# Optimization experiments

Measured on AMD Instinct MI355X. Metric: run time of the kernel, lower is better.

Reference implementation:

```python
import jax, jax.numpy as jnp
import numpy as np

N_HEAD = 8
HID = 256
V_DIM = HID // N_HEAD
IN_CH = 3
OUT_CH = 1
N_BLOCKS = 4
BATCH = 4
N_FULL = 4096
N_LAT = 1024
LOCALITIES = (3.0, 5.0, 5.0, 5.0, 5.0, 3.0)


def _linear(x, w, b):
    # eqx.nn.Linear convention: w is [out, in]
    return x @ w.T + b


def _pos_att(m_dist, x, r, weight, locality):
    # m_dist: [h, Nq, Nk]; x: [b, Nk, HID]; r: [h,1,1]; weight: [h, HID, V_DIM]
    scale = jnp.tan(0.25 * jnp.pi * (1 - 1e-07) * (1 + jnp.sin(r)))  # [h,1,1]
    sd = m_dist * scale  # [h, Nq, Nk]
    if locality <= 100:
        thr = jnp.percentile(sd, locality, axis=-1, keepdims=True)
        sd = jnp.where(sd <= thr, sd, jnp.inf)
    att = jax.nn.softmax(-sd, axis=-1)  # [h, Nq, Nk]
    value = jnp.einsum('bnj,hjk->bhnk', x, weight)  # [b, h, Nk, V_DIM]
    out = jnp.einsum('hjn,bhnk->bhjk', att, value)  # [b, h, Nq, V_DIM]
    out = out.transpose(0, 2, 1, 3).reshape(out.shape[0], out.shape[2], -1)  # [b, Nq, HID]
    return jax.nn.gelu(out)


def setup_inputs():
    key = jax.random.key(0)
    ks = jax.random.split(key, 16)
    def nrm(k, shape, scale=1.0):
        return jax.random.normal(k, shape, dtype=jnp.float32) * scale
    inv = float(1.0 / np.sqrt(HID))
    return {
        'x': nrm(ks[0], (BATCH, N_FULL, IN_CH)),
        'm_dist_down': jax.random.uniform(ks[1], (N_HEAD, N_LAT, N_FULL), dtype=jnp.float32),
        'm_dist_blocks': jax.random.uniform(ks[2], (N_BLOCKS, N_HEAD, N_LAT, N_LAT), dtype=jnp.float32),
        'm_dist_up': jax.random.uniform(ks[3], (N_HEAD, N_FULL, N_LAT), dtype=jnp.float32),
        'en_w': nrm(ks[4], (HID, IN_CH), float(1.0 / np.sqrt(IN_CH))),
        'en_b': jnp.zeros((HID,), jnp.float32),
        'down_r': nrm(ks[5], (N_HEAD, 1, 1)),
        'down_w': nrm(ks[6], (N_HEAD, HID, V_DIM), inv),
        'pa_r': nrm(ks[7], (N_BLOCKS, N_HEAD, 1, 1)),
        'pa_w': nrm(ks[8], (N_BLOCKS, N_HEAD, HID, V_DIM), inv),
        'mlp1_w': nrm(ks[9], (N_BLOCKS, HID, HID), inv),
        'mlp1_b': jnp.zeros((N_BLOCKS, HID), jnp.float32),
        'mlp2_w': nrm(ks[10], (N_BLOCKS, HID, HID), inv),
        'mlp2_b': jnp.zeros((N_BLOCKS, HID), jnp.float32),
        'res_w': nrm(ks[11], (N_BLOCKS, HID, HID), inv),
        'res_b': jnp.zeros((N_BLOCKS, HID), jnp.float32),
        'up_r': nrm(ks[12], (N_HEAD, 1, 1)),
        'up_w': nrm(ks[13], (N_HEAD, HID, V_DIM), inv),
        'de1_w': nrm(ks[14], (HID, HID), inv),
        'de1_b': jnp.zeros((HID,), jnp.float32),
        'de2_w': nrm(ks[15], (OUT_CH, HID), inv),
        'de2_b': jnp.zeros((OUT_CH,), jnp.float32),
    }


def reference(x, m_dist_down, m_dist_blocks, m_dist_up, en_w, en_b, down_r, down_w,
              pa_r, pa_w, mlp1_w, mlp1_b, mlp2_w, mlp2_b, res_w, res_b,
              up_r, up_w, de1_w, de1_b, de2_w, de2_b):
    # Encoder: lift + downsampling position-attention
    h = jax.nn.gelu(_linear(x, en_w, en_b))  # [b, N_FULL, HID]
    h = _pos_att(m_dist_down, h, down_r, down_w, LOCALITIES[0])  # [b, N_LAT, HID]
    # Processor blocks: PA -> MLP, plus linear residual, gelu
    for i in range(N_BLOCKS):
        pa = _pos_att(m_dist_blocks[i], h, pa_r[i], pa_w[i], LOCALITIES[1 + i])
        mlp = _linear(jax.nn.gelu(_linear(pa, mlp1_w[i], mlp1_b[i])), mlp2_w[i], mlp2_b[i])
        h = jax.nn.gelu(mlp + _linear(h, res_w[i], res_b[i]))
    # Decoder: upsampling position-attention + projection
    h = _pos_att(m_dist_up, h, up_r, up_w, LOCALITIES[-1])  # [b, N_FULL, HID]
    h = jax.nn.gelu(_linear(h, de1_w, de1_b))
    return _linear(h, de2_w, de2_b)  # [b, N_FULL, OUT_CH]
```

## Files before the change

### kernel.cpp

```cpp
#include <hip/hip_runtime.h>
#include <math.h>


typedef short bf16x8 __attribute__((ext_vector_type(8)));
typedef float f32x4 __attribute__((ext_vector_type(4)));

__device__ __forceinline__ float gelu_f(float x) {
  float x3 = x * x * x;
  float inner = x + 0.044715f * x3;
  float t = tanhf(0.7978845608028654f * inner);
  return x * (0.5f * (1.0f + t));
}

__device__ __forceinline__ unsigned short f2bf(float x) {
  union { float f; unsigned u; } v; v.f = x;
  return (unsigned short)((v.u + 0x7fffu + ((v.u >> 16) & 1u)) >> 16);
}
__device__ __forceinline__ float bf2f(unsigned short b) {
  union { unsigned u; float f; } v; v.u = ((unsigned)b) << 16; return v.f;
}
__device__ __forceinline__ void store_bf(unsigned short* hi, unsigned short* lo,
                                         size_t i, float v) {
  unsigned short h = f2bf(v);
  hi[i] = h;
  lo[i] = f2bf(v - bf2f(h));
}

struct PrepArgs {
  const float *mlp1, *mlp2, *res, *de1, *down, *pa, *up;
  const float *down_r, *pa_r, *up_r;
  unsigned short *rm_hi, *rm_lo, *val_hi, *val_lo;
  float* scales;
};
__global__ __launch_bounds__(256) void k_prep(PrepArgs p) {
  if (blockIdx.x == 4864) {
    int t = threadIdx.x;
    if (t >= 48) return;
    float rv;
    if (t < 8) rv = p.down_r[t];
    else if (t < 40) rv = p.pa_r[t - 8];
    else rv = p.up_r[t - 40];
    double rd = (double)rv;
    float s1 = (float)sin(rd);
    float u = 1.0f + s1;
    float vc = (float)(0.7853981633974483 * (1.0 - 1e-7));
    float wf = vc * u;
    p.scales[t] = (float)tan((double)wf);
    return;
  }
  int i = blockIdx.x * 256 + threadIdx.x;
  if (i < 851968) {
    const float* src; int off;
    if (i < 262144)      { src = p.mlp1; off = i; }
    else if (i < 524288) { src = p.mlp2; off = i - 262144; }
    else if (i < 786432) { src = p.res;  off = i - 524288; }
    else                 { src = p.de1;  off = i - 786432; }
    float x = src[off];
    store_bf(p.rm_hi, p.rm_lo, i, x);
  } else if (i < 1245184) {
    int ii = i - 851968;
    const float* src; int off;
    if (ii < 65536)       { src = p.down; off = ii; }
    else if (ii < 327680) { src = p.pa;   off = ii - 65536; }
    else                  { src = p.up;   off = ii - 327680; }
    int m = off >> 16, rem = off & 65535;
    int o = rem >> 8, j = rem & 255;
    float x = src[(size_t)m * 65536 + (o >> 5) * 8192 + j * 32 + (o & 31)];
    store_bf(p.val_hi, p.val_lo, ii, x);
  }
}

__global__ __launch_bounds__(256) void k_lift(const float* __restrict__ x,
                                              const float* __restrict__ w,
                                              const float* __restrict__ b,
                                              unsigned short* __restrict__ ohi,
                                              unsigned short* __restrict__ olo) {
  int gid = blockIdx.x * 256 + threadIdx.x;
  int m = gid >> 8, o = gid & 255;
  float a0 = x[m * 3 + 0], a1 = x[m * 3 + 1], a2 = x[m * 3 + 2];
  float acc = a0 * w[o * 3 + 0] + a1 * w[o * 3 + 1] + a2 * w[o * 3 + 2] + b[o];
  store_bf(ohi, olo, gid, gelu_f(acc));
}

template <int ACT, int ADDRES, int OBF16>
__global__ __launch_bounds__(256) void k_gemm(
    const unsigned short* __restrict__ Ahi, const unsigned short* __restrict__ Alo,
    const unsigned short* __restrict__ Whi, const unsigned short* __restrict__ Wlo,
    const float* __restrict__ bias, const float* __restrict__ D,
    float* __restrict__ C, unsigned short* __restrict__ Chi,
    unsigned short* __restrict__ Clo) {
  int t = threadIdx.x;
  int w = t >> 6, l = t & 63;
  int m0 = blockIdx.x * 64 + (w >> 1) * 32;
  int o0 = blockIdx.y * 64 + (w & 1) * 32;
  int fr = l & 15, fq = l >> 4;
  f32x4 acc[2][2] = {};
  size_t a0 = (size_t)(m0 + fr) * 256 + fq * 8;
  size_t a1 = a0 + 16 * 256;
  size_t b0 = (size_t)(o0 + fr) * 256 + fq * 8;
  size_t b1 = b0 + 16 * 256;
#define MFMA4(ACC, AH, AL, BH, BL)                                            \
  ACC = __builtin_amdgcn_mfma_f32_16x16x32_bf16(AH, BH, ACC, 0, 0, 0);        \
  ACC = __builtin_amdgcn_mfma_f32_16x16x32_bf16(AH, BL, ACC, 0, 0, 0);        \
  ACC = __builtin_amdgcn_mfma_f32_16x16x32_bf16(AL, BH, ACC, 0, 0, 0);        \
  ACC = __builtin_amdgcn_mfma_f32_16x16x32_bf16(AL, BL, ACC, 0, 0, 0);
  for (int ks = 0; ks < 8; ++ks) {
    int k0 = ks * 32;
    bf16x8 A0h = *(const bf16x8*)(Ahi + a0 + k0);
    bf16x8 A0l = *(const bf16x8*)(Alo + a0 + k0);
    bf16x8 A1h = *(const bf16x8*)(Ahi + a1 + k0);
    bf16x8 A1l = *(const bf16x8*)(Alo + a1 + k0);
    bf16x8 B0h = *(const bf16x8*)(Whi + b0 + k0);
    bf16x8 B0l = *(const bf16x8*)(Wlo + b0 + k0);
    bf16x8 B1h = *(const bf16x8*)(Whi + b1 + k0);
    bf16x8 B1l = *(const bf16x8*)(Wlo + b1 + k0);
    MFMA4(acc[0][0], A0h, A0l, B0h, B0l)
    MFMA4(acc[0][1], A0h, A0l, B1h, B1l)
    MFMA4(acc[1][0], A1h, A1l, B0h, B0l)
    MFMA4(acc[1][1], A1h, A1l, B1h, B1l)
  }
  float bb[2];
  bb[0] = bias ? bias[o0 + fr] : 0.0f;
  bb[1] = bias ? bias[o0 + 16 + fr] : 0.0f;
#pragma unroll
  for (int i = 0; i < 2; ++i) {
#pragma unroll
    for (int jx = 0; jx < 2; ++jx) {
      int col = o0 + jx * 16 + fr;
#pragma unroll
      for (int r = 0; r < 4; ++r) {
        int rowi = m0 + i * 16 + fq * 4 + r;
        size_t oidx = (size_t)rowi * 256 + col;
        float v = acc[i][jx][r] + bb[jx];
        if (ADDRES) v += D[oidx];
        if (ACT) v = gelu_f(v);
        if (OBF16) store_bf(Chi, Clo, oidx, v);
        else C[oidx] = v;
      }
    }
  }
}

__global__ __launch_bounds__(256) void k_gemm2(
    const unsigned short* __restrict__ A1hi, const unsigned short* __restrict__ A1lo,
    const unsigned short* __restrict__ W1hi, const unsigned short* __restrict__ W1lo,
    const unsigned short* __restrict__ A2hi, const unsigned short* __restrict__ A2lo,
    const unsigned short* __restrict__ W2hi, const unsigned short* __restrict__ W2lo,
    const float* __restrict__ b1, const float* __restrict__ b2,
    unsigned short* __restrict__ Chi, unsigned short* __restrict__ Clo) {
  int t = threadIdx.x;
  int w = t >> 6, l = t & 63;
  int m0 = blockIdx.x * 64 + (w >> 1) * 32;
  int o0 = blockIdx.y * 64 + (w & 1) * 32;
  int fr = l & 15, fq = l >> 4;
  f32x4 acc[2][2] = {};
  size_t a0 = (size_t)(m0 + fr) * 256 + fq * 8;
  size_t a1 = a0 + 16 * 256;
  size_t b0 = (size_t)(o0 + fr) * 256 + fq * 8;
  size_t b1o = b0 + 16 * 256;
  for (int ks = 0; ks < 8; ++ks) {
    int k0 = ks * 32;
    {
      bf16x8 A0h = *(const bf16x8*)(A1hi + a0 + k0);
      bf16x8 A0l = *(const bf16x8*)(A1lo + a0 + k0);
      bf16x8 A1h_ = *(const bf16x8*)(A1hi + a1 + k0);
      bf16x8 A1l_ = *(const bf16x8*)(A1lo + a1 + k0);
      bf16x8 B0h = *(const bf16x8*)(W1hi + b0 + k0);
      bf16x8 B0l = *(const bf16x8*)(W1lo + b0 + k0);
      bf16x8 B1h = *(const bf16x8*)(W1hi + b1o + k0);
      bf16x8 B1l = *(const bf16x8*)(W1lo + b1o + k0);
      MFMA4(acc[0][0], A0h, A0l, B0h, B0l)
      MFMA4(acc[0][1], A0h, A0l, B1h, B1l)
      MFMA4(acc[1][0], A1h_, A1l_, B0h, B0l)
      MFMA4(acc[1][1], A1h_, A1l_, B1h, B1l)
    }
    {
      bf16x8 A0h = *(const bf16x8*)(A2hi + a0 + k0);
      bf16x8 A0l = *(const bf16x8*)(A2lo + a0 + k0);
      bf16x8 A1h_ = *(const bf16x8*)(A2hi + a1 + k0);
      bf16x8 A1l_ = *(const bf16x8*)(A2lo + a1 + k0);
      bf16x8 B0h = *(const bf16x8*)(W2hi + b0 + k0);
      bf16x8 B0l = *(const bf16x8*)(W2lo + b0 + k0);
      bf16x8 B1h = *(const bf16x8*)(W2hi + b1o + k0);
      bf16x8 B1l = *(const bf16x8*)(W2lo + b1o + k0);
      MFMA4(acc[0][0], A0h, A0l, B0h, B0l)
      MFMA4(acc[0][1], A0h, A0l, B1h, B1l)
      MFMA4(acc[1][0], A1h_, A1l_, B0h, B0l)
      MFMA4(acc[1][1], A1h_, A1l_, B1h, B1l)
    }
  }
#undef MFMA4
  float bb[2];
  bb[0] = b1[o0 + fr] + b2[o0 + fr];
  bb[1] = b1[o0 + 16 + fr] + b2[o0 + 16 + fr];
#pragma unroll
  for (int i = 0; i < 2; ++i) {
#pragma unroll
    for (int jx = 0; jx < 2; ++jx) {
      int col = o0 + jx * 16 + fr;
#pragma unroll
      for (int r = 0; r < 4; ++r) {
        int rowi = m0 + i * 16 + fq * 4 + r;
        size_t oidx = (size_t)rowi * 256 + col;
        store_bf(Chi, Clo, oidx, gelu_f(acc[i][jx][r] + bb[jx]));
      }
    }
  }
}

template <int N, int CAP, int MW>
__global__ __launch_bounds__(256, MW) void k_wselpv(
    const float* __restrict__ mdist, const float* __restrict__ scales,
    int sc_off, int Nq, int k_lo, float hw, float lw, float frac,
    const float* __restrict__ V, int Nk,
    unsigned short* __restrict__ out_hi, unsigned short* __restrict__ out_lo) {
  constexpr int CH = N / 256;
  constexpr int SMAX = (CAP + 63) / 64;
  __shared__ float cv[4][CAP];
  __shared__ int ci[4][CAP];
  __shared__ int ccnt[4];
  __shared__ float svsel[4][2];
  __shared__ float swin[4][32];

  int tid = threadIdx.x;
  int w = tid >> 6, l = tid & 63;
  int row = blockIdx.x * 4 + w;
  int h = row / Nq, j = row - h * Nq;
  float scale = scales[sc_off + h];
  const float4* mrow4 = (const float4*)(mdist + (size_t)row * N);

  float4 s0 = mrow4[l];
  float smin = fminf(fminf(s0.x, s0.y), fminf(s0.z, s0.w));
  float smax = fmaxf(fmaxf(s0.x, s0.y), fmaxf(s0.z, s0.w));
#pragma unroll
  for (int off = 32; off > 0; off >>= 1) {
    smin = fminf(smin, __shfl_xor(smin, off));
    smax = fmaxf(smax, __shfl_xor(smax, off));
  }
  float est = smin + (smax - smin) * frac;

  if (l == 0) ccnt[w] = 0;
  float lmin = INFINITY, lmax = -INFINITY;
#pragma unroll 4
  for (int e = 0; e < CH; ++e) {
    float4 v = mrow4[l + 64 * e];
    lmin = fminf(lmin, fminf(fminf(v.x, v.y), fminf(v.z, v.w)));
    lmax = fmaxf(lmax, fmaxf(fmaxf(v.x, v.y), fmaxf(v.z, v.w)));
    int i0 = 4 * (l + 64 * e);
    if (v.x < est) { int p = atomicAdd(&ccnt[w], 1); if (p < CAP) { cv[w][p] = v.x; ci[w][p] = i0; } }
    if (v.y < est) { int p = atomicAdd(&ccnt[w], 1); if (p < CAP) { cv[w][p] = v.y; ci[w][p] = i0 + 1; } }
    if (v.z < est) { int p = atomicAdd(&ccnt[w], 1); if (p < CAP) { cv[w][p] = v.z; ci[w][p] = i0 + 2; } }
    if (v.w < est) { int p = atomicAdd(&ccnt[w], 1); if (p < CAP) { cv[w][p] = v.w; ci[w][p] = i0 + 3; } }
  }
#pragma unroll
  for (int off = 32; off > 0; off >>= 1) {
    lmin = fminf(lmin, __shfl_xor(lmin, off));
    lmax = fmaxf(lmax, __shfl_xor(lmax, off));
  }
  float rmin = lmin, rmax = lmax;

  int K = 0;
  float inv_total = 1.0f;
  if (rmax > rmin) {
    float range = rmax - rmin;
    float margin = fmaxf(fabsf(rmax) * 1e-6f, 1e-30f);
    float rtop = rmax + margin;
    float wtop = est;
    bool have = true;
    if (!(wtop > rmin)) {
      wtop = rmin + range * frac;
      if (!(wtop > rmin)) wtop = rtop;
      have = false;
    }
    int attempt = 0;
    float v_lo = rmin, v_hi = rmin;
    int count = 0;
    float xv[SMAX];
    for (int it = 0; it < 20; ++it) {
      if (!have) {
        if (l == 0) ccnt[w] = 0;
#pragma unroll 4
        for (int e = 0; e < CH; ++e) {
          float4 v = mrow4[l + 64 * e];
          int i0 = 4 * (l + 64 * e);
          if (v.x < wtop) { int p = atomicAdd(&ccnt[w], 1); if (p < CAP) { cv[w][p] = v.x; ci[w][p] = i0; } }
          if (v.y < wtop) { int p = atomicAdd(&ccnt[w], 1); if (p < CAP) { cv[w][p] = v.y; ci[w][p] = i0 + 1; } }
          if (v.z < wtop) { int p = atomicAdd(&ccnt[w], 1); if (p < CAP) { cv[w][p] = v.z; ci[w][p] = i0 + 2; } }
          if (v.w < wtop) { int p = atomicAdd(&ccnt[w], 1); if (p < CAP) { cv[w][p] = v.w; ci[w][p] = i0 + 3; } }
        }
        have = true;
      }
      count = ccnt[w];
      if (count < k_lo + 2) {
        wtop = (attempt == 0) ? (rmin + range * frac)
                              : fminf(rmin + (wtop - rmin) * 3.0f, rtop);
        if (!(wtop > rmin)) wtop = rtop;
        attempt++; have = false; continue;
      }
      if (count > CAP) {
        float fw = rmin + range * frac;
        float sw = rmin + (wtop - rmin) * 0.6f;
        wtop = (attempt == 0) ? fminf(fw, sw) : sw;
        attempt++; have = false; continue;
      }

#pragma unroll
      for (int s = 0; s < SMAX; ++s) {
        int slot = l + 64 * s;
        xv[s] = (slot < count) ? cv[w][slot] : INFINITY;
      }
      float wlo = rmin, whi = wtop;
      int rbase = 0, cntw = count;
      int found = 0, degen = 0;
      for (int bs = 0; bs < 32; ++bs) {
        if (cntw <= 24) break;
        float mid = 0.5f * (wlo + whi);
        if (!(mid > wlo && mid < whi)) { degen = 1; break; }
        int c4 = 0;
#pragma unroll
        for (int s = 0; s < SMAX; ++s) c4 += (xv[s] >= wlo && xv[s] < mid) ? 1 : 0;
#pragma unroll
        for (int off = 32; off > 0; off >>= 1) c4 += __shfl_xor(c4, off);
        int rrel = k_lo - rbase;
        if (rrel + 1 < c4) { whi = mid; cntw = c4; }
        else if (rrel >= c4) { wlo = mid; rbase += c4; cntw -= c4; }
        else {
          float mx = -INFINITY, mn = INFINITY;
#pragma unroll
          for (int s = 0; s < SMAX; ++s) {
            float v = xv[s];
            if (v >= wlo && v < mid) mx = fmaxf(mx, v);
            if (v >= mid && v < whi) mn = fminf(mn, v);
          }
#pragma unroll
          for (int off = 32; off > 0; off >>= 1) {
            mx = fmaxf(mx, __shfl_xor(mx, off));
            mn = fminf(mn, __shfl_xor(mn, off));
          }
          v_lo = mx; v_hi = mn; found = 1;
          break;
        }
      }
      if (!found) {
        if (!degen && cntw <= 32) {
          if (l == 0) ccnt[w] = 0;
#pragma unroll
          for (int s = 0; s < SMAX; ++s) {
            float v = xv[s];
            if (v >= wlo && v < whi) {
              int p = atomicAdd(&ccnt[w], 1);
              if (p < 32) swin[w][p] = v;
            }
          }
          int m = ccnt[w];
          if (m > 32) m = 32;
          float myv = (l < m) ? swin[w][l] : INFINITY;
          int clt = 0, ceq = 0;
          for (int jj = 0; jj < m; ++jj) {
            float y = swin[w][jj];
            clt += (y < myv) ? 1 : 0;
            ceq += (y == myv) ? 1 : 0;
          }
          int rr = k_lo - rbase;
          if (l < m) {
            if (clt <= rr && rr < clt + ceq) svsel[w][0] = myv;
            if (clt <= rr + 1 && rr + 1 < clt + ceq) svsel[w][1] = myv;
          }
          v_lo = svsel[w][0];
          v_hi = svsel[w][1];
          if (l == 0) ccnt[w] = count;
        } else {
          int clt[SMAX], ceq[SMAX];
#pragma unroll
          for (int s = 0; s < SMAX; ++s) { clt[s] = 0; ceq[s] = 0; }
          for (int jj = 0; jj < count; ++jj) {
            float y = cv[w][jj];
#pragma unroll
            for (int s = 0; s < SMAX; ++s) {
              clt[s] += (y < xv[s]) ? 1 : 0;
              ceq[s] += (y == xv[s]) ? 1 : 0;
            }
          }
#pragma unroll
          for (int s = 0; s < SMAX; ++s) {
            int slot = l + 64 * s;
            if (slot < count) {
              if (clt[s] <= k_lo && k_lo < clt[s] + ceq[s]) svsel[w][0] = xv[s];
              if (clt[s] <= k_lo + 1 && k_lo + 1 < clt[s] + ceq[s]) svsel[w][1] = xv[s];
            }
          }
          v_lo = svsel[w][0];
          v_hi = svsel[w][1];
        }
      }
      float vlos0 = __fmul_rn(v_lo, scale);
      float vhis0 = __fmul_rn(v_hi, scale);
      float thr0 = __fadd_rn(__fmul_rn(vlos0, lw), __fmul_rn(vhis0, hw));
      if (__fmul_rn(wtop, scale) <= thr0) {
        wtop = fminf(rmin + (wtop - rmin) * 3.0f, rtop);
        attempt++; have = false; continue;
      }
      break;
    }

    float vlos = __fmul_rn(v_lo, scale);
    float vhis = __fmul_rn(v_hi, scale);
    float thr = __fadd_rn(__fmul_rn(vlos, lw), __fmul_rn(vhis, hw));
    float rmins = __fmul_rn(rmin, scale);

    int oi[SMAX]; int kp[SMAX];
#pragma unroll
    for (int s = 0; s < SMAX; ++s) {
      int slot = l + 64 * s;
      oi[s] = 0; kp[s] = 0;
      if (slot < count) {
        oi[s] = ci[w][slot];
        kp[s] = (__fmul_rn(xv[s], scale) <= thr) ? 1 : 0;
      }
    }
    int base = 0;
    float lsum = 0.0f;
    unsigned long long mlt = (l == 0) ? 0ull : (~0ull >> (64 - l));
#pragma unroll
    for (int s = 0; s < SMAX; ++s) {
      unsigned long long bal = __ballot(kp[s] != 0);
      int pos = base + (int)__popcll(bal & mlt);
      if (kp[s]) {
        float e0 = expf(__fsub_rn(rmins, __fmul_rn(xv[s], scale)));
        cv[w][pos] = e0;
        ci[w][pos] = oi[s];
        lsum += e0;
      }
      base += (int)__popcll(bal);
    }
    K = base;
#pragma unroll
    for (int off = 32; off > 0; off >>= 1) lsum += __shfl_xor(lsum, off);
    inv_total = 1.0f / lsum;
  } else {
    K = 0;
    inv_total = 1.0f / (float)Nk;
  }

  int b = l >> 4, c4 = (l & 15) * 2;
  int hcol = h * 32 + c4;
  const float* Vb = V + (size_t)b * Nk * 256;
  float acc0 = 0.0f, acc1 = 0.0f;
  if (K > 0) {
    for (int e = 0; e < K; ++e) {
      float we = cv[w][e];
      int n = ci[w][e];
      const float2 vv = *(const float2*)(Vb + (size_t)n * 256 + hcol);
      acc0 = fmaf(we, vv.x, acc0);
      acc1 = fmaf(we, vv.y, acc1);
    }
  } else {
    for (int n = 0; n < Nk; ++n) {
      const float2 vv = *(const float2*)(Vb + (size_t)n * 256 + hcol);
      acc0 += vv.x;
      acc1 += vv.y;
    }
  }
  size_t oidx = ((size_t)b * Nq + j) * 256 + hcol;
  store_bf(out_hi, out_lo, oidx, gelu_f(acc0 * inv_total));
  store_bf(out_hi, out_lo, oidx + 1, gelu_f(acc1 * inv_total));
}

__global__ __launch_bounds__(256) void k_de2(const float* __restrict__ A,
                                             const float* __restrict__ w,
                                             const float* __restrict__ b,
                                             float* __restrict__ out) {
  int t = threadIdx.x;
  int row = blockIdx.x * 4 + (t >> 6);
  int lane = t & 63;
  const float* ar = A + (size_t)row * 256;
  float s = 0.0f;
  for (int i = lane; i < 256; i += 64) s = fmaf(ar[i], w[i], s);
#pragma unroll
  for (int off = 32; off > 0; off >>= 1) s += __shfl_down(s, off);
  if (lane == 0) out[row] = s + b[0];
}

struct SelParams { int k_lo; float hw, lw, frac; };
static SelParams sel_params(double q, int N) {
  SelParams p;
  float idx_q = (float)(q / 100.0);
  float pos = idx_q * (float)(N - 1);
  float lo = floorf(pos);
  p.k_lo = (int)lo;
  p.hw = pos - lo;
  p.lw = 1.0f - p.hw;
  float need = (float)(p.k_lo + 2);
  p.frac = (need + 6.0f * sqrtf(need) + 8.0f) / (float)N;
  return p;
}

extern "C" void kernel_launch(void* const* d_in, const int* in_sizes, int n_in,
                              void* d_out, int out_size, void* d_ws, size_t ws_size,
                              hipStream_t stream) {
  const float* x      = (const float*)d_in[0];
  const float* mdd    = (const float*)d_in[1];
  const float* mdb    = (const float*)d_in[2];
  const float* mdu    = (const float*)d_in[3];
  const float* en_w   = (const float*)d_in[4];
  const float* en_b   = (const float*)d_in[5];
  const float* down_r = (const float*)d_in[6];
  const float* down_w = (const float*)d_in[7];
  const float* pa_r   = (const float*)d_in[8];
  const float* pa_w   = (const float*)d_in[9];
  const float* mlp1_w = (const float*)d_in[10];
  const float* mlp1_b = (const float*)d_in[11];
  const float* mlp2_w = (const float*)d_in[12];
  const float* mlp2_b = (const float*)d_in[13];
  const float* res_w  = (const float*)d_in[14];
  const float* res_b  = (const float*)d_in[15];
  const float* up_r   = (const float*)d_in[16];
  const float* up_w   = (const float*)d_in[17];
  const float* de1_w  = (const float*)d_in[18];
  const float* de1_b  = (const float*)d_in[19];
  const float* de2_w  = (const float*)d_in[20];
  const float* de2_b  = (const float*)d_in[21];
  float* out = (float*)d_out;
  char* base = (char*)d_ws;

  float* val               = (float*)base;
  unsigned short* hB_hi    = (unsigned short*)(base + 16777216);
  unsigned short* hB_lo    = (unsigned short*)(base + 18874368);
  unsigned short* hfull_hi = (unsigned short*)(base + 20971520);
  unsigned short* hfull_lo = (unsigned short*)(base + 29360128);
  unsigned short* paout_hi = (unsigned short*)(base + 37748736);
  unsigned short* paout_lo = (unsigned short*)(base + 46137344);
  unsigned short* hA_hi    = (unsigned short*)(base + 54525952);
  unsigned short* hA_lo    = (unsigned short*)(base + 56623104);
  unsigned short* t1_hi    = (unsigned short*)(base + 58720256);
  unsigned short* t1_lo    = (unsigned short*)(base + 60817408);
  unsigned short* wrm_hi   = (unsigned short*)(base + 62914560);
  unsigned short* wrm_lo   = (unsigned short*)(base + 64618496);
  unsigned short* wval_hi  = (unsigned short*)(base + 66322432);
  unsigned short* wval_lo  = (unsigned short*)(base + 67108864);
  float* scales            = (float*)(base + 67895296);

  PrepArgs pa;
  pa.mlp1 = mlp1_w; pa.mlp2 = mlp2_w; pa.res = res_w; pa.de1 = de1_w;
  pa.down = down_w; pa.pa = pa_w; pa.up = up_w;
  pa.down_r = down_r; pa.pa_r = pa_r; pa.up_r = up_r;
  pa.rm_hi = wrm_hi; pa.rm_lo = wrm_lo; pa.val_hi = wval_hi; pa.val_lo = wval_lo;
  pa.scales = scales;
  k_prep<<<4865, 256, 0, stream>>>(pa);

  k_lift<<<16384, 256, 0, stream>>>(x, en_w, en_b, hfull_hi, hfull_lo);

  SelParams pd = sel_params(3.0, 4096);
  k_gemm<0, 0, 0><<<dim3(256, 4), 256, 0, stream>>>(
      hfull_hi, hfull_lo, wval_hi, wval_lo, nullptr, nullptr, val, nullptr, nullptr);
  k_wselpv<4096, 256, 4><<<2048, 256, 0, stream>>>(
      mdd, scales, 0, 1024, pd.k_lo, pd.hw, pd.lw, pd.frac, val, 4096, hA_hi, hA_lo);

  SelParams pb = sel_params(5.0, 1024);
  for (int i = 0; i < 4; i++) {
    unsigned short* in_hi  = (i & 1) ? hB_hi : hA_hi;
    unsigned short* in_lo  = (i & 1) ? hB_lo : hA_lo;
    unsigned short* out_hi = (i & 1) ? hA_hi : hB_hi;
    unsigned short* out_lo = (i & 1) ? hA_lo : hB_lo;
    k_gemm<0, 0, 0><<<dim3(64, 4), 256, 0, stream>>>(
        in_hi, in_lo, wval_hi + 65536 + i * 65536, wval_lo + 65536 + i * 65536,
        nullptr, nullptr, val, nullptr, nullptr);
    k_wselpv<1024, 256, 8><<<2048, 256, 0, stream>>>(
        mdb + (size_t)i * 8388608, scales, 8 + i * 8, 1024, pb.k_lo, pb.hw, pb.lw,
        pb.frac, val, 1024, paout_hi, paout_lo);
    k_gemm<1, 0, 1><<<dim3(64, 4), 256, 0, stream>>>(
        paout_hi, paout_lo, wrm_hi + i * 65536, wrm_lo + i * 65536,
        mlp1_b + i * 256, nullptr, nullptr, t1_hi, t1_lo);
    k_gemm2<<<dim3(64, 4), 256, 0, stream>>>(
        t1_hi, t1_lo, wrm_hi + 262144 + i * 65536, wrm_lo + 262144 + i * 65536,
        in_hi, in_lo, wrm_hi + 524288 + i * 65536, wrm_lo + 524288 + i * 65536,
        mlp2_b + i * 256, res_b + i * 256, out_hi, out_lo);
  }

  SelParams pu = sel_params(3.0, 1024);
  k_gemm<0, 0, 0><<<dim3(64, 4), 256, 0, stream>>>(
      hA_hi, hA_lo, wval_hi + 327680, wval_lo + 327680, nullptr, nullptr,
      val, nullptr, nullptr);
  k_wselpv<1024, 192, 8><<<8192, 256, 0, stream>>>(
      mdu, scales, 40, 4096, pu.k_lo, pu.hw, pu.lw, pu.frac, val, 1024,
      paout_hi, paout_lo);

  k_gemm<1, 0, 0><<<dim3(256, 4), 256, 0, stream>>>(
      paout_hi, paout_lo, wrm_hi + 786432, wrm_lo + 786432, de1_b, nullptr,
      val, nullptr, nullptr);
  k_de2<<<4096, 256, 0, stream>>>(val, de2_w, de2_b, out);
}
```

Measured before the change: 521.7 us.

## Process each attention row with a whole block instead of one wavefront

Replaces the per-wavefront row selection kernel with a block-per-row version. All four wavefronts scan a quarter of the row, collect candidates into per-wave segments, wave 0 does the percentile search, and the weighted value gather is split across waves and reduced through shared memory. The initial candidate fraction margin is also tightened, which makes candidate sets smaller but may trigger more retry passes. The change adds block-wide barriers and runs 4x more blocks, and wave 0 becomes a serial bottleneck during selection.

```diff
diff --git a/kernel.cpp b/kernel.cpp
--- a/kernel.cpp
+++ b/kernel.cpp
@@ -208,262 +208,252 @@
   }
 }
 
-template <int N, int CAP, int MW>
-__global__ __launch_bounds__(256, MW) void k_wselpv(
+template <int N>
+__global__ __launch_bounds__(256, 8) void k_bselpv(
     const float* __restrict__ mdist, const float* __restrict__ scales,
     int sc_off, int Nq, int k_lo, float hw, float lw, float frac,
     const float* __restrict__ V, int Nk,
     unsigned short* __restrict__ out_hi, unsigned short* __restrict__ out_lo) {
-  constexpr int CH = N / 256;
-  constexpr int SMAX = (CAP + 63) / 64;
-  __shared__ float cv[4][CAP];
-  __shared__ int ci[4][CAP];
+  constexpr int CH = N / 1024;
+  constexpr int SEG = 64;
+  constexpr int CAP = 256;
+  __shared__ float cv[CAP];
+  __shared__ int ci[CAP];
   __shared__ int ccnt[4];
-  __shared__ float svsel[4][2];
-  __shared__ float swin[4][32];
-
-  int tid = threadIdx.x;
-  int w = tid >> 6, l = tid & 63;
-  int row = blockIdx.x * 4 + w;
+  __shared__ float sminmax[8];
+  __shared__ float svsel[2];
+  __shared__ float swin[32];
+  __shared__ int sgc;
+  __shared__ int sK;
+  __shared__ float sinv;
+  __shared__ int sflag;
+  __shared__ float2 pacc[256];
+
+  int t = threadIdx.x;
+  int w = t >> 6, l = t & 63;
+  int row = blockIdx.x;
   int h = row / Nq, j = row - h * Nq;
   float scale = scales[sc_off + h];
   const float4* mrow4 = (const float4*)(mdist + (size_t)row * N);
 
-  float4 s0 = mrow4[l];
-  float smin = fminf(fminf(s0.x, s0.y), fminf(s0.z, s0.w));
-  float smax = fmaxf(fmaxf(s0.x, s0.y), fmaxf(s0.z, s0.w));
-#pragma unroll
-  for (int off = 32; off > 0; off >>= 1) {
-    smin = fminf(smin, __shfl_xor(smin, off));
-    smax = fmaxf(smax, __shfl_xor(smax, off));
-  }
-  float est = smin + (smax - smin) * frac;
-
-  if (l == 0) ccnt[w] = 0;
   float lmin = INFINITY, lmax = -INFINITY;
-#pragma unroll 4
+#pragma unroll
   for (int e = 0; e < CH; ++e) {
-    float4 v = mrow4[l + 64 * e];
+    float4 v = mrow4[t + 256 * e];
     lmin = fminf(lmin, fminf(fminf(v.x, v.y), fminf(v.z, v.w)));
     lmax = fmaxf(lmax, fmaxf(fmaxf(v.x, v.y), fmaxf(v.z, v.w)));
-    int i0 = 4 * (l + 64 * e);
-    if (v.x < est) { int p = atomicAdd(&ccnt[w], 1); if (p < CAP) { cv[w][p] = v.x; ci[w][p] = i0; } }
-    if (v.y < est) { int p = atomicAdd(&ccnt[w], 1); if (p < CAP) { cv[w][p] = v.y; ci[w][p] = i0 + 1; } }
-    if (v.z < est) { int p = atomicAdd(&ccnt[w], 1); if (p < CAP) { cv[w][p] = v.z; ci[w][p] = i0 + 2; } }
-    if (v.w < est) { int p = atomicAdd(&ccnt[w], 1); if (p < CAP) { cv[w][p] = v.w; ci[w][p] = i0 + 3; } }
   }
 #pragma unroll
   for (int off = 32; off > 0; off >>= 1) {
     lmin = fminf(lmin, __shfl_xor(lmin, off));
     lmax = fmaxf(lmax, __shfl_xor(lmax, off));
   }
-  float rmin = lmin, rmax = lmax;
+  if (l == 0) { sminmax[w] = lmin; sminmax[4 + w] = lmax; }
+  __syncthreads();
+  float rmin = fminf(fminf(sminmax[0], sminmax[1]), fminf(sminmax[2], sminmax[3]));
+  float rmax = fmaxf(fmaxf(sminmax[4], sminmax[5]), fmaxf(sminmax[6], sminmax[7]));
 
   int K = 0;
-  float inv_total = 1.0f;
+  float inv_total = 1.0f / (float)Nk;
   if (rmax > rmin) {
     float range = rmax - rmin;
     float margin = fmaxf(fabsf(rmax) * 1e-6f, 1e-30f);
     float rtop = rmax + margin;
-    float wtop = est;
-    bool have = true;
-    if (!(wtop > rmin)) {
-      wtop = rmin + range * frac;
-      if (!(wtop > rmin)) wtop = rtop;
-      have = false;
-    }
-    int attempt = 0;
-    float v_lo = rmin, v_hi = rmin;
-    int count = 0;
-    float xv[SMAX];
+    float wtop = rmin + range * frac;
+    if (!(wtop > rmin)) wtop = rtop;
     for (int it = 0; it < 20; ++it) {
-      if (!have) {
-        if (l == 0) ccnt[w] = 0;
-#pragma unroll 4
-        for (int e = 0; e < CH; ++e) {
-          float4 v = mrow4[l + 64 * e];
-          int i0 = 4 * (l + 64 * e);
-          if (v.x < wtop) { int p = atomicAdd(&ccnt[w], 1); if (p < CAP) { cv[w][p] = v.x; ci[w][p] = i0; } }
-          if (v.y < wtop) { int p = atomicAdd(&ccnt[w], 1); if (p < CAP) { cv[w][p] = v.y; ci[w][p] = i0 + 1; } }
-          if (v.z < wtop) { int p = atomicAdd(&ccnt[w], 1); if (p < CAP) { cv[w][p] = v.z; ci[w][p] = i0 + 2; } }
-          if (v.w < wtop) { int p = atomicAdd(&ccnt[w], 1); if (p < CAP) { cv[w][p] = v.w; ci[w][p] = i0 + 3; } }
+      if (l == 0) ccnt[w] = 0;
+      __syncthreads();
+#pragma unroll
+      for (int e = 0; e < CH; ++e) {
+        float4 v = mrow4[t + 256 * e];
+        int i0 = 4 * (t + 256 * e);
+        if (v.x < wtop) { int p = atomicAdd(&ccnt[w], 1); if (p < SEG) { cv[w * SEG + p] = v.x; ci[w * SEG + p] = i0; } }
+        if (v.y < wtop) { int p = atomicAdd(&ccnt[w], 1); if (p < SEG) { cv[w * SEG + p] = v.y; ci[w * SEG + p] = i0 + 1; } }
+        if (v.z < wtop) { int p = atomicAdd(&ccnt[w], 1); if (p < SEG) { cv[w * SEG + p] = v.z; ci[w * SEG + p] = i0 + 2; } }
+        if (v.w < wtop) { int p = atomicAdd(&ccnt[w], 1); if (p < SEG) { cv[w * SEG + p] = v.w; ci[w * SEG + p] = i0 + 3; } }
+      }
+      __syncthreads();
+      int cs0 = ccnt[0], cs1 = ccnt[1], cs2 = ccnt[2], cs3 = ccnt[3];
+      int total = cs0 + cs1 + cs2 + cs3;
+      bool ovf = (cs0 > SEG) || (cs1 > SEG) || (cs2 > SEG) || (cs3 > SEG);
+      if (total < k_lo + 2) {
+        wtop = fminf(rmin + (wtop - rmin) * 3.0f, rtop);
+        continue;
+      }
+      if (ovf) {
+        wtop = rmin + (wtop - rmin) * 0.6f;
+        continue;
+      }
+      if (w == 0) {
+        int cnts[4] = {cs0, cs1, cs2, cs3};
+        float xv[4];
+        int oi[4];
+        int inseg[4];
+#pragma unroll
+        for (int s = 0; s < 4; ++s) {
+          inseg[s] = (l < cnts[s]) ? 1 : 0;
+          xv[s] = inseg[s] ? cv[s * SEG + l] : INFINITY;
+          oi[s] = inseg[s] ? ci[s * SEG + l] : 0;
         }
-        have = true;
-      }
-      count = ccnt[w];
-      if (count < k_lo + 2) {
-        wtop = (attempt == 0) ? (rmin + range * frac)
-                              : fminf(rmin + (wtop - rmin) * 3.0f, rtop);
-        if (!(wtop > rmin)) wtop = rtop;
-        attempt++; have = false; continue;
-      }
-      if (count > CAP) {
-        float fw = rmin + range * frac;
-        float sw = rmin + (wtop - rmin) * 0.6f;
-        wtop = (attempt == 0) ? fminf(fw, sw) : sw;
-        attempt++; have = false; continue;
-      }
-
-#pragma unroll
-      for (int s = 0; s < SMAX; ++s) {
-        int slot = l + 64 * s;
-        xv[s] = (slot < count) ? cv[w][slot] : INFINITY;
-      }
-      float wlo = rmin, whi = wtop;
-      int rbase = 0, cntw = count;
-      int found = 0, degen = 0;
-      for (int bs = 0; bs < 32; ++bs) {
-        if (cntw <= 24) break;
-        float mid = 0.5f * (wlo + whi);
-        if (!(mid > wlo && mid < whi)) { degen = 1; break; }
-        int c4 = 0;
-#pragma unroll
-        for (int s = 0; s < SMAX; ++s) c4 += (xv[s] >= wlo && xv[s] < mid) ? 1 : 0;
-#pragma unroll
-        for (int off = 32; off > 0; off >>= 1) c4 += __shfl_xor(c4, off);
-        int rrel = k_lo - rbase;
-        if (rrel + 1 < c4) { whi = mid; cntw = c4; }
-        else if (rrel >= c4) { wlo = mid; rbase += c4; cntw -= c4; }
-        else {
-          float mx = -INFINITY, mn = INFINITY;
-#pragma unroll
-          for (int s = 0; s < SMAX; ++s) {
-            float v = xv[s];
-            if (v >= wlo && v < mid) mx = fmaxf(mx, v);
-            if (v >= mid && v < whi) mn = fminf(mn, v);
+        float v_lo = rmin, v_hi = rmin;
+        float wlo = rmin, whi = wtop;
+        int rbase = 0, cntw = total;
+        int found = 0, degen = 0;
+        for (int bs = 0; bs < 32; ++bs) {
+          if (cntw <= 24) break;
+          float mid = 0.5f * (wlo + whi);
+          if (!(mid > wlo && mid < whi)) { degen = 1; break; }
+          int c4 = 0;
+#pragma unroll
+          for (int s = 0; s < 4; ++s) c4 += (xv[s] >= wlo && xv[s] < mid) ? 1 : 0;
+#pragma unroll
+          for (int off = 32; off > 0; off >>= 1) c4 += __shfl_xor(c4, off);
+          int rrel = k_lo - rbase;
+          if (rrel + 1 < c4) { whi = mid; cntw = c4; }
+          else if (rrel >= c4) { wlo = mid; rbase += c4; cntw -= c4; }
+          else {
+            float mx = -INFINITY, mn = INFINITY;
+#pragma unroll
+            for (int s = 0; s < 4; ++s) {
+              float v = xv[s];
+              if (v >= wlo && v < mid) mx = fmaxf(mx, v);
+              if (v >= mid && v < whi) mn = fminf(mn, v);
+            }
+#pragma unroll
+            for (int off = 32; off > 0; off >>= 1) {
+              mx = fmaxf(mx, __shfl_xor(mx, off));
+              mn = fminf(mn, __shfl_xor(mn, off));
+            }
+            v_lo = mx; v_hi = mn; found = 1;
+            break;
           }
-#pragma unroll
-          for (int off = 32; off > 0; off >>= 1) {
-            mx = fmaxf(mx, __shfl_xor(mx, off));
-            mn = fminf(mn, __shfl_xor(mn, off));
+        }
+        if (!found) {
+          if (!degen && cntw <= 32) {
+            if (l == 0) sgc = 0;
+#pragma unroll
+            for (int s = 0; s < 4; ++s) {
+              float v = xv[s];
+              if (v >= wlo && v < whi) {
+                int p = atomicAdd(&sgc, 1);
+                if (p < 32) swin[p] = v;
+              }
+            }
+            int m = sgc;
+            if (m > 32) m = 32;
+            float myv = (l < m) ? swin[l] : INFINITY;
+            int clt = 0, ceq = 0;
+            for (int jj = 0; jj < m; ++jj) {
+              float y = swin[jj];
+              clt += (y < myv) ? 1 : 0;
+              ceq += (y == myv) ? 1 : 0;
+            }
+            int rr = k_lo - rbase;
+            if (l < m) {
+              if (clt <= rr && rr < clt + ceq) svsel[0] = myv;
+              if (clt <= rr + 1 && rr + 1 < clt + ceq) svsel[1] = myv;
+            }
+            v_lo = svsel[0];
+            v_hi = svsel[1];
+          } else {
+            int clt[4], ceq[4];
+#pragma unroll
+            for (int s = 0; s < 4; ++s) { clt[s] = 0; ceq[s] = 0; }
+            for (int sj = 0; sj < 4; ++sj) {
+              int cs = cnts[sj];
+              for (int jj = 0; jj < cs; ++jj) {
+                float y = cv[sj * SEG + jj];
+#pragma unroll
+                for (int s = 0; s < 4; ++s) {
+                  clt[s] += (y < xv[s]) ? 1 : 0;
+                  ceq[s] += (y == xv[s]) ? 1 : 0;
+                }
+              }
+            }
+#pragma unroll
+            for (int s = 0; s < 4; ++s) {
+              if (inseg[s]) {
+                if (clt[s] <= k_lo && k_lo < clt[s] + ceq[s]) svsel[0] = xv[s];
+                if (clt[s] <= k_lo + 1 && k_lo + 1 < clt[s] + ceq[s]) svsel[1] = xv[s];
+              }
+            }
+            v_lo = svsel[0];
+            v_hi = svsel[1];
           }
-          v_lo = mx; v_hi = mn; found = 1;
-          break;
         }
-      }
-      if (!found) {
-        if (!degen && cntw <= 32) {
-          if (l == 0) ccnt[w] = 0;
-#pragma unroll
-          for (int s = 0; s < SMAX; ++s) {
-            float v = xv[s];
-            if (v >= wlo && v < whi) {
-              int p = atomicAdd(&ccnt[w], 1);
-              if (p < 32) swin[w][p] = v;
-            }
+        float vlos = __fmul_rn(v_lo, scale);
+        float vhis = __fmul_rn(v_hi, scale);
+        float thr = __fadd_rn(__fmul_rn(vlos, lw), __fmul_rn(vhis, hw));
+        float rmins = __fmul_rn(rmin, scale);
+        if (__fmul_rn(wtop, scale) <= thr) {
+          if (l == 0) sflag = 1;
+        } else {
+          if (l == 0) sflag = 0;
+          int kp[4];
+#pragma unroll
+          for (int s = 0; s < 4; ++s)
+            kp[s] = inseg[s] ? ((__fmul_rn(xv[s], scale) <= thr) ? 1 : 0) : 0;
+          int base = 0;
+          float lsum = 0.0f;
+          unsigned long long mlt = (l == 0) ? 0ull : (~0ull >> (64 - l));
+#pragma unroll
+          for (int s = 0; s < 4; ++s) {
+            unsigned long long bal = __ballot(kp[s] != 0);
+            int pos = base + (int)__popcll(bal & mlt);
+            if (kp[s]) {
+              float e0 = expf(__fsub_rn(rmins, __fmul_rn(xv[s], scale)));
+              cv[pos] = e0;
+              ci[pos] = oi[s];
+              lsum += e0;
+            }
+            base += (int)__popcll(bal);
           }
-          int m = ccnt[w];
-          if (m > 32) m = 32;
-          float myv = (l < m) ? swin[w][l] : INFINITY;
-          int clt = 0, ceq = 0;
-          for (int jj = 0; jj < m; ++jj) {
-            float y = swin[w][jj];
-            clt += (y < myv) ? 1 : 0;
-            ceq += (y == myv) ? 1 : 0;
-          }
-          int rr = k_lo - rbase;
-          if (l < m) {
-            if (clt <= rr && rr < clt + ceq) svsel[w][0] = myv;
-            if (clt <= rr + 1 && rr + 1 < clt + ceq) svsel[w][1] = myv;
-          }
-          v_lo = svsel[w][0];
-          v_hi = svsel[w][1];
-          if (l == 0) ccnt[w] = count;
-        } else {
-          int clt[SMAX], ceq[SMAX];
-#pragma unroll
-          for (int s = 0; s < SMAX; ++s) { clt[s] = 0; ceq[s] = 0; }
-          for (int jj = 0; jj < count; ++jj) {
-            float y = cv[w][jj];
-#pragma unroll
-            for (int s = 0; s < SMAX; ++s) {
-              clt[s] += (y < xv[s]) ? 1 : 0;
-              ceq[s] += (y == xv[s]) ? 1 : 0;
-            }
-          }
-#pragma unroll
-          for (int s = 0; s < SMAX; ++s) {
-            int slot = l + 64 * s;
-            if (slot < count) {
-              if (clt[s] <= k_lo && k_lo < clt[s] + ceq[s]) svsel[w][0] = xv[s];
-              if (clt[s] <= k_lo + 1 && k_lo + 1 < clt[s] + ceq[s]) svsel[w][1] = xv[s];
-            }
-          }
-          v_lo = svsel[w][0];
-          v_hi = svsel[w][1];
+#pragma unroll
+          for (int off = 32; off > 0; off >>= 1) lsum += __shfl_xor(lsum, off);
+          if (l == 0) { sK = base; sinv = 1.0f / lsum; }
         }
       }
-      float vlos0 = __fmul_rn(v_lo, scale);
-      float vhis0 = __fmul_rn(v_hi, scale);
-      float thr0 = __fadd_rn(__fmul_rn(vlos0, lw), __fmul_rn(vhis0, hw));
-      if (__fmul_rn(wtop, scale) <= thr0) {
+      __syncthreads();
+      if (sflag) {
         wtop = fminf(rmin + (wtop - rmin) * 3.0f, rtop);
-        attempt++; have = false; continue;
-      }
+        continue;
+      }
+      K = sK;
+      inv_total = sinv;
       break;
     }
-
-    float vlos = __fmul_rn(v_lo, scale);
-    float vhis = __fmul_rn(v_hi, scale);
-    float thr = __fadd_rn(__fmul_rn(vlos, lw), __fmul_rn(vhis, hw));
-    float rmins = __fmul_rn(rmin, scale);
-
-    int oi[SMAX]; int kp[SMAX];
-#pragma unroll
-    for (int s = 0; s < SMAX; ++s) {
-      int slot = l + 64 * s;
-      oi[s] = 0; kp[s] = 0;
-      if (slot < count) {
-        oi[s] = ci[w][slot];
-        kp[s] = (__fmul_rn(xv[s], scale) <= thr) ? 1 : 0;
-      }
-    }
-    int base = 0;
-    float lsum = 0.0f;
-    unsigned long long mlt = (l == 0) ? 0ull : (~0ull >> (64 - l));
-#pragma unroll
-    for (int s = 0; s < SMAX; ++s) {
-      unsigned long long bal = __ballot(kp[s] != 0);
-      int pos = base + (int)__popcll(bal & mlt);
-      if (kp[s]) {
-        float e0 = expf(__fsub_rn(rmins, __fmul_rn(xv[s], scale)));
-        cv[w][pos] = e0;
-        ci[w][pos] = oi[s];
-        lsum += e0;
-      }
-      base += (int)__popcll(bal);
-    }
-    K = base;
-#pragma unroll
-    for (int off = 32; off > 0; off >>= 1) lsum += __shfl_xor(lsum, off);
-    inv_total = 1.0f / lsum;
-  } else {
-    K = 0;
-    inv_total = 1.0f / (float)Nk;
-  }
-
-  int b = l >> 4, c4 = (l & 15) * 2;
-  int hcol = h * 32 + c4;
+  }
+
+  int b = (t >> 4) & 3, c2 = t & 15;
+  int hcol = h * 32 + c2 * 2;
   const float* Vb = V + (size_t)b * Nk * 256;
   float acc0 = 0.0f, acc1 = 0.0f;
   if (K > 0) {
-    for (int e = 0; e < K; ++e) {
-      float we = cv[w][e];
-      int n = ci[w][e];
+    for (int e = w; e < K; e += 4) {
+      float we = cv[e];
+      int n = ci[e];
       const float2 vv = *(const float2*)(Vb + (size_t)n * 256 + hcol);
       acc0 = fmaf(we, vv.x, acc0);
       acc1 = fmaf(we, vv.y, acc1);
     }
-  } else {
-    for (int n = 0; n < Nk; ++n) {
+  } else if (rmax <= rmin) {
+    for (int n = w; n < Nk; n += 4) {
       const float2 vv = *(const float2*)(Vb + (size_t)n * 256 + hcol);
       acc0 += vv.x;
       acc1 += vv.y;
     }
   }
-  size_t oidx = ((size_t)b * Nq + j) * 256 + hcol;
-  store_bf(out_hi, out_lo, oidx, gelu_f(acc0 * inv_total));
-  store_bf(out_hi, out_lo, oidx + 1, gelu_f(acc1 * inv_total));
+  pacc[t] = make_float2(acc0, acc1);
+  __syncthreads();
+  if (t < 64) {
+    float2 p0 = pacc[t], p1 = pacc[64 + t], p2 = pacc[128 + t], p3 = pacc[192 + t];
+    float r0 = ((p0.x + p1.x) + (p2.x + p3.x)) * inv_total;
+    float r1 = ((p0.y + p1.y) + (p2.y + p3.y)) * inv_total;
+    size_t oidx = ((size_t)b * Nq + j) * 256 + hcol;
+    store_bf(out_hi, out_lo, oidx, gelu_f(r0));
+    store_bf(out_hi, out_lo, oidx + 1, gelu_f(r1));
+  }
 }
 
 __global__ __launch_bounds__(256) void k_de2(const float* __restrict__ A,
@@ -491,7 +481,7 @@
   p.hw = pos - lo;
   p.lw = 1.0f - p.hw;
   float need = (float)(p.k_lo + 2);
-  p.frac = (need + 6.0f * sqrtf(need) + 8.0f) / (float)N;
+  p.frac = (need + 2.5f * sqrtf(need) + 8.0f) / (float)N;
   return p;
 }
 
@@ -553,7 +543,7 @@
   SelParams pd = sel_params(3.0, 4096);
   k_gemm<0, 0, 0><<<dim3(256, 4), 256, 0, stream>>>(
       hfull_hi, hfull_lo, wval_hi, wval_lo, nullptr, nullptr, val, nullptr, nullptr);
-  k_wselpv<4096, 256, 4><<<2048, 256, 0, stream>>>(
+  k_bselpv<4096><<<8192, 256, 0, stream>>>(
       mdd, scales, 0, 1024, pd.k_lo, pd.hw, pd.lw, pd.frac, val, 4096, hA_hi, hA_lo);
 
   SelParams pb = sel_params(5.0, 1024);
@@ -565,7 +555,7 @@
     k_gemm<0, 0, 0><<<dim3(64, 4), 256, 0, stream>>>(
         in_hi, in_lo, wval_hi + 65536 + i * 65536, wval_lo + 65536 + i * 65536,
         nullptr, nullptr, val, nullptr, nullptr);
-    k_wselpv<1024, 256, 8><<<2048, 256, 0, stream>>>(
+    k_bselpv<1024><<<8192, 256, 0, stream>>>(
         mdb + (size_t)i * 8388608, scales, 8 + i * 8, 1024, pb.k_lo, pb.hw, pb.lw,
         pb.frac, val, 1024, paout_hi, paout_lo);
     k_gemm<1, 0, 1><<<dim3(64, 4), 256, 0, stream>>>(
@@ -581,7 +571,7 @@
   k_gemm<0, 0, 0><<<dim3(64, 4), 256, 0, stream>>>(
       hA_hi, hA_lo, wval_hi + 327680, wval_lo + 327680, nullptr, nullptr,
       val, nullptr, nullptr);
-  k_wselpv<1024, 192, 8><<<8192, 256, 0, stream>>>(
+  k_bselpv<1024><<<32768, 256, 0, stream>>>(
       mdu, scales, 40, 4096, pu.k_lo, pu.hw, pu.lw, pu.frac, val, 1024,
       paout_hi, paout_lo);
 
```

Measured after the change: 657.8 us. 26.1% more time.
